# Performance work log

Measured on AMD Instinct MI355X. Metric: run time of the kernel, lower is better.

## Reference

```python
import jax, jax.numpy as jnp
import numpy as np

B, S, D_IN, D_CODE, K = 8, 4096, 1024, 64, 4096


def setup_inputs() -> dict:
    key = jax.random.key(0)
    k1, k2, k3, k4 = jax.random.split(key, 4)
    return {
        "input": jax.random.normal(k1, (B, S, D_IN), dtype=jnp.float32),
        "W_send": jax.random.normal(k2, (D_IN, D_CODE), dtype=jnp.float32) * (1.0 / np.sqrt(D_IN)),
        "b_send": jnp.zeros((D_CODE,), dtype=jnp.float32),
        "emb": jax.random.normal(k3, (K, D_CODE), dtype=jnp.float32),
        "W_recv": jax.random.normal(k4, (D_CODE, D_IN), dtype=jnp.float32) * (1.0 / np.sqrt(D_CODE)),
        "b_recv": jnp.zeros((D_IN,), dtype=jnp.float32),
    }


def reference(input, W_send, b_send, emb, W_recv, b_recv):
    # encoder: z = send(input) -> [B, S, D_CODE]
    z = jnp.einsum('bsi,ic->bsc', input, W_send) + b_send

    # VQEmbedding.lookup: argmin_k ||e_k||^2 - 2 <z, e_k>  (no-grad path)
    sqr = jnp.sum(emb * emb, axis=1)                      # [K]
    cov = jnp.einsum('bsc,kc->bsk', z, emb)               # [B, S, K]
    indices = jnp.argmin(sqr - 2.0 * cov, axis=-1)        # [B, S] int

    # fetch embeddings (gather)
    vectors = emb[indices]                                # [B, S, D_CODE]

    # straight-through estimator: values = z + sg(vectors - z)
    values = z + jax.lax.stop_gradient(vectors - z)

    # decoder: x = recv(values) -> [B, S, D_IN]
    x = jnp.einsum('bsc,ci->bsi', values, W_recv) + b_recv

    # VQEmbedding.loss (reduction='sum')
    embedding_loss = jnp.sum((vectors - jax.lax.stop_gradient(z)) ** 2)
    commitment_loss = jnp.sum((z - jax.lax.stop_gradient(vectors)) ** 2)

    # empirical code entropy in bits
    num_codes = emb.shape[0]
    counts = jnp.bincount(indices.ravel(), length=num_codes)
    p = counts.astype(jnp.float32) / jnp.float32(indices.size)
    ent = -jnp.sum(jnp.where(p > 0, p * jnp.log(jnp.where(p > 0, p, 1.0)), 0.0)) / jnp.log(2.0)

    return x, indices, embedding_loss, commitment_loss, ent
```

## Files before the change

kernel.cpp:

```cpp
#include <hip/hip_runtime.h>

#define DIN 1024
#define DC 64
#define KC 4096

typedef _Float16 f16x8 __attribute__((ext_vector_type(8)));
typedef _Float16 f16x4 __attribute__((ext_vector_type(4)));
typedef float f32x4 __attribute__((ext_vector_type(4)));

__device__ __forceinline__ void gll16(const void* g, void* l) {
    __builtin_amdgcn_global_load_lds(
        (const __attribute__((address_space(1))) unsigned int*)g,
        (__attribute__((address_space(3))) unsigned int*)l, 16, 0, 0);
}

__global__ __launch_bounds__(256) void k_prep(const float* __restrict__ emb,
                                              const float* __restrict__ Ws,
                                              const float* __restrict__ Wr,
                                              _Float16* __restrict__ Ee,
                                              float* __restrict__ sqr,
                                              _Float16* __restrict__ Wh,
                                              _Float16* __restrict__ WrT,
                                              int* __restrict__ counts) {
    int b = blockIdx.x;
    int tid = threadIdx.x;
    if (b < 1024) {
        int code = b * 4 + (tid >> 6);
        int lane = tid & 63;
        float v = emb[(size_t)code * DC + lane];
        Ee[(size_t)code * 64 + lane] = (_Float16)v;
        float s = v * v;
        #pragma unroll
        for (int m = 1; m < 64; m <<= 1) s += __shfl_xor(s, m);
        if (lane == 0) sqr[code] = s;
        if (tid < 4) counts[b * 4 + tid] = 0;
        return;
    }
    if (b < 1040) {
        int k0 = (b - 1024) * 64;
        #pragma unroll
        for (int it = 0; it < 16; ++it) {
            int q = it * 256 + tid;
            int c = q >> 6, kl = q & 63;
            float v = Ws[(size_t)(k0 + kl) * 64 + c];
            Wh[(size_t)c * 1024 + k0 + kl] = (_Float16)v;
        }
        return;
    }
    int b2 = b - 1040;
    #pragma unroll
    for (int it = 0; it < 16; ++it) {
        int k = it * 4 + (tid >> 6);
        int rr = b2 * 64 + (tid & 63);
        WrT[(size_t)rr * 64 + k] = (_Float16)Wr[(size_t)k * 1024 + rr];
    }
}

__global__ __launch_bounds__(256) void k_main(const float* __restrict__ in,
                                              const _Float16* __restrict__ Wh,
                                              const float* __restrict__ bs,
                                              const _Float16* __restrict__ Ee,
                                              const float* __restrict__ sqr,
                                              int* __restrict__ idx,
                                              float* __restrict__ out_idx,
                                              int* __restrict__ counts,
                                              float* __restrict__ lpart) {
    __shared__ char smem[32768];
    const int tid = threadIdx.x;
    const int row0 = blockIdx.x * 64;
    const int wid = tid >> 6, lane = tid & 63;
    const int c15 = lane & 15, g = lane >> 4;
    const int g16 = g * 16;
    const int wm = wid >> 1, wn = wid & 1;

    f32x4 acc[2][2];
    const f32x4 zz4 = {0.f, 0.f, 0.f, 0.f};
    #pragma unroll
    for (int mf = 0; mf < 2; ++mf)
        #pragma unroll
        for (int nf = 0; nf < 2; ++nf) acc[mf][nf] = zz4;

    int abyte[2], aswz[2], bbyte[2], bswz[2];
    #pragma unroll
    for (int mf = 0; mf < 2; ++mf) {
        int r = wm * 32 + mf * 16 + c15;
        abyte[mf] = r * 128; aswz[mf] = (r & 7) << 4;
    }
    #pragma unroll
    for (int nf = 0; nf < 2; ++nf) {
        int c = wn * 32 + nf * 16 + c15;
        bbyte[nf] = c * 128; bswz[nf] = (c & 7) << 4;
    }

    auto stageB = [&](int buf, int s) {
        char* dst = smem + buf * 16384 + 8192;
        #pragma unroll
        for (int r = 0; r < 2; ++r) {
            int p = r * 4096 + wid * 1024 + lane * 16;
            int row = p >> 7, off = p & 127;
            int soff = off ^ ((row & 7) << 4);
            gll16((const char*)Wh + (size_t)row * 2048 + s * 128 + soff,
                  dst + p);
        }
    };
    auto loadA = [&](int s, float4* a) {
        #pragma unroll
        for (int it = 0; it < 4; ++it) {
            int q = it * 256 + tid;
            int r = q >> 4, c4 = q & 15;
            a[it] = *(const float4*)&in[(size_t)(row0 + r) * DIN + s * 64 + c4 * 4];
        }
    };
    auto writeA = [&](int buf, const float4* a) {
        char* Ah = smem + buf * 16384;
        #pragma unroll
        for (int it = 0; it < 4; ++it) {
            int q = it * 256 + tid;
            int r = q >> 4, c4 = q & 15;
            float v[4] = {a[it].x, a[it].y, a[it].z, a[it].w};
            f16x4 h;
            #pragma unroll
            for (int j = 0; j < 4; ++j) h[j] = (_Float16)v[j];
            int o = r * 128 + ((c4 * 8) ^ ((r & 7) << 4));
            *(f16x4*)(Ah + o) = h;
        }
    };
    auto compute = [&](int buf) {
        const char* Ah = smem + buf * 16384;
        const char* Bh = Ah + 8192;
        #pragma unroll
        for (int ks = 0; ks < 2; ++ks) {
            int koff = ks * 64 + g16;
            f16x8 bh[2];
            #pragma unroll
            for (int nf = 0; nf < 2; ++nf)
                bh[nf] = *(const f16x8*)(Bh + bbyte[nf] + (koff ^ bswz[nf]));
            #pragma unroll
            for (int mf = 0; mf < 2; ++mf) {
                f16x8 ah = *(const f16x8*)(Ah + abyte[mf] + (koff ^ aswz[mf]));
                #pragma unroll
                for (int nf = 0; nf < 2; ++nf)
                    acc[mf][nf] = __builtin_amdgcn_mfma_f32_16x16x32_f16(
                        ah, bh[nf], acc[mf][nf], 0, 0, 0);
            }
        }
    };

    {
        float4 a0[4];
        loadA(0, a0);
        stageB(0, 0);
        writeA(0, a0);
    }
    __syncthreads();
    for (int s = 0; s < 16; ++s) {
        int c = s & 1;
        float4 an[4];
        if (s < 15) {
            loadA(s + 1, an);
            stageB(c ^ 1, s + 1);
        }
        compute(c);
        if (s < 15) writeA(c ^ 1, an);
        __syncthreads();
    }

    char* Zt = smem + 16384;
    #pragma unroll
    for (int nf = 0; nf < 2; ++nf) {
        int k = wn * 32 + nf * 16 + c15;
        float bias = bs[k];
        #pragma unroll
        for (int mf = 0; mf < 2; ++mf)
            #pragma unroll
            for (int r2 = 0; r2 < 4; ++r2) {
                int row = wm * 32 + mf * 16 + g * 4 + r2;
                _Float16 zh = (_Float16)(acc[mf][nf][r2] + bias);
                *(_Float16*)(Zt + row * 128 + ((k * 2) ^ ((row & 7) << 4))) = zh;
            }
    }
    __syncthreads();

    const int wm2 = wm, wn2 = wn;
    f16x8 zfh[2][2];
    #pragma unroll
    for (int nf = 0; nf < 2; ++nf) {
        int zr = wn2 * 32 + nf * 16 + c15;
        int sw = (zr & 7) << 4;
        #pragma unroll
        for (int j = 0; j < 2; ++j)
            zfh[j][nf] = *(const f16x8*)(Zt + zr * 128 + ((j * 64 + g16) ^ sw));
    }

    int rbase[2], rx[2];
    #pragma unroll
    for (int mf = 0; mf < 2; ++mf) {
        int r = wm2 * 32 + mf * 16 + c15;
        rbase[mf] = r * 128;
        rx[mf] = (r & 7) << 4;
    }

    auto stageE = [&](int ch, int buf) {
        char* dst = smem + buf * 8192;
        const char* src = (const char*)Ee + (size_t)ch * 8192;
        #pragma unroll
        for (int t = 0; t < 2; ++t) {
            int p = t * 4096 + tid * 16;
            int r = p >> 7, off = p & 127;
            gll16(src + r * 128 + (off ^ ((r & 7) << 4)), dst + p);
        }
    };

    float bv[2];
    int   bi[2];
    #pragma unroll
    for (int nf = 0; nf < 2; ++nf) { bv[nf] = 3.402823466e38f; bi[nf] = 0; }

    stageE(0, 0);
    __syncthreads();

    for (int ch = 0; ch < 64; ++ch) {
        const int buf = ch & 1;
        f32x4 sqv[2];
        #pragma unroll
        for (int mf = 0; mf < 2; ++mf)
            sqv[mf] = *(const f32x4*)(sqr + ch * 64 + wm2 * 32 + mf * 16 + g * 4);

        if (ch < 63) stageE(ch + 1, buf ^ 1);

        const char* base = smem + buf * 8192;
        f32x4 sacc[2][2];
        #pragma unroll
        for (int j = 0; j < 2; ++j) {
            const int kbyte = j * 64 + g16;
            f16x8 af[2];
            #pragma unroll
            for (int mf = 0; mf < 2; ++mf)
                af[mf] = *(const f16x8*)(base + rbase[mf] + (kbyte ^ rx[mf]));
            #pragma unroll
            for (int mf = 0; mf < 2; ++mf)
                #pragma unroll
                for (int nf = 0; nf < 2; ++nf)
                    sacc[mf][nf] = __builtin_amdgcn_mfma_f32_16x16x32_f16(
                        af[mf], zfh[j][nf],
                        j == 0 ? zz4 : sacc[mf][nf], 0, 0, 0);
        }

        #pragma unroll
        for (int nf = 0; nf < 2; ++nf) {
            #pragma unroll
            for (int mf = 0; mf < 2; ++mf) {
                f32x4 v = sqv[mf] - sacc[mf][nf] * 2.0f;
                #pragma unroll
                for (int r2 = 0; r2 < 4; ++r2) {
                    if (v[r2] < bv[nf]) {
                        bv[nf] = v[r2];
                        bi[nf] = ch * 64 + wm2 * 32 + mf * 16 + g * 4 + r2;
                    }
                }
            }
        }
        __syncthreads();
    }

    float* redv = (float*)(smem + 24576);
    int*   redi = (int*)(smem + 25088);
    float* zsqa = (float*)(smem + 25600);

    #pragma unroll
    for (int nf = 0; nf < 2; ++nf) {
        float v_ = bv[nf]; int i_ = bi[nf];
        #pragma unroll
        for (int m = 16; m <= 32; m <<= 1) {
            float ov = __shfl_xor(v_, m);
            int oi = __shfl_xor(i_, m);
            if (ov < v_ || (ov == v_ && oi < i_)) { v_ = ov; i_ = oi; }
        }
        if (g == 0) {
            int rl = wn2 * 32 + nf * 16 + c15;
            redv[wm2 * 64 + rl] = v_;
            redi[wm2 * 64 + rl] = i_;
        }
    }
    if (wm2 == 0) {
        #pragma unroll
        for (int nf = 0; nf < 2; ++nf) {
            float s = 0.f;
            #pragma unroll
            for (int j = 0; j < 2; ++j)
                #pragma unroll
                for (int e = 0; e < 8; ++e) {
                    float zv = (float)zfh[j][nf][e];
                    s += zv * zv;
                }
            s += __shfl_xor(s, 16);
            s += __shfl_xor(s, 32);
            if (g == 0) zsqa[wn2 * 32 + nf * 16 + c15] = s;
        }
    }
    __syncthreads();
    if (tid < 64) {
        float v0 = redv[tid]; int i0 = redi[tid];
        float v1 = redv[64 + tid]; int i1 = redi[64 + tid];
        if (v1 < v0 || (v1 == v0 && i1 < i0)) { v0 = v1; i0 = i1; }
        int grow = row0 + tid;
        idx[grow] = i0;
        out_idx[grow] = (float)i0;
        atomicAdd(&counts[i0], 1);
        float lossv = v0 + zsqa[tid];
        #pragma unroll
        for (int m = 1; m < 64; m <<= 1) lossv += __shfl_xor(lossv, m);
        if (tid == 0) lpart[blockIdx.x] = lossv;
    }
}

__global__ __launch_bounds__(256) void k_recv(const _Float16* __restrict__ Ee,
                                              const _Float16* __restrict__ WrT,
                                              const float* __restrict__ br,
                                              const int* __restrict__ idx,
                                              const int* __restrict__ counts,
                                              const float* __restrict__ lpart,
                                              float* __restrict__ x,
                                              float* __restrict__ out_sc) {
    __shared__ char smem[24832];
    int tid = threadIdx.x;

    if (blockIdx.x == 512) {
        float* red = (float*)smem;
        red[tid] = lpart[tid] + lpart[256 + tid];
        __syncthreads();
        for (int s = 128; s > 0; s >>= 1) {
            if (tid < s) red[tid] += red[tid + s];
            __syncthreads();
        }
        float loss = red[0];
        __syncthreads();
        float ep = 0.f;
        for (int k = tid; k < KC; k += 256) {
            int c = counts[k];
            if (c > 0) {
                float p = (float)c / 32768.0f;
                ep += p * logf(p);
            }
        }
        red[tid] = ep; __syncthreads();
        for (int s = 128; s > 0; s >>= 1) {
            if (tid < s) red[tid] += red[tid + s];
            __syncthreads();
        }
        if (tid == 0) {
            out_sc[0] = loss;
            out_sc[1] = loss;
            out_sc[2] = -red[0] * 1.4426950408889634f;
        }
        return;
    }

    const int row0 = blockIdx.x * 64;
    const int wid = tid >> 6, lane = tid & 63;
    const int c15 = lane & 15, g = lane >> 4;
    const int g16 = g * 16;
    int* sidx = (int*)(smem + 24576);

    if (tid < 64) sidx[tid] = idx[row0 + tid];
    __syncthreads();

    #pragma unroll
    for (int t = 0; t < 2; ++t) {
        int p = t * 4096 + tid * 16;
        int r = p >> 7, off = p & 127;
        gll16((const char*)Ee + (size_t)sidx[r] * 128 + (off ^ ((r & 7) << 4)),
              smem + p);
    }

    auto stageW = [&](int cc, int buf) {
        char* dst = smem + 8192 + buf * 8192;
        #pragma unroll
        for (int t = 0; t < 2; ++t) {
            int p = t * 4096 + tid * 16;
            int r = p >> 7, off = p & 127;
            gll16((const char*)WrT + (size_t)(cc * 64 + r) * 128
                      + (off ^ ((r & 7) << 4)),
                  dst + p);
        }
    };
    stageW(0, 0);
    __syncthreads();

    int abase[4], ax[4];
    #pragma unroll
    for (int mf = 0; mf < 4; ++mf) {
        int r = mf * 16 + c15;
        abase[mf] = r * 128;
        ax[mf] = (r & 7) << 4;
    }
    const int brow = wid * 16 + c15;
    const int bbase = 8192 + brow * 128;
    const int bx = (brow & 7) << 4;

    const f32x4 zz4 = {0.f, 0.f, 0.f, 0.f};
    for (int cc = 0; cc < 16; ++cc) {
        const int buf = cc & 1;
        if (cc < 15) stageW(cc + 1, buf ^ 1);

        const int col = cc * 64 + wid * 16 + c15;
        float bias = br[col];

        f32x4 acc[4];
        #pragma unroll
        for (int j = 0; j < 2; ++j) {
            const int kbyte = j * 64 + g16;
            f16x8 bf = *(const f16x8*)(smem + buf * 8192 + bbase + (kbyte ^ bx));
            #pragma unroll
            for (int mf = 0; mf < 4; ++mf) {
                f16x8 af = *(const f16x8*)(smem + abase[mf] + (kbyte ^ ax[mf]));
                acc[mf] = __builtin_amdgcn_mfma_f32_16x16x32_f16(
                    af, bf, j == 0 ? zz4 : acc[mf], 0, 0, 0);
            }
        }

        #pragma unroll
        for (int mf = 0; mf < 4; ++mf)
            #pragma unroll
            for (int r2 = 0; r2 < 4; ++r2)
                x[(size_t)(row0 + mf * 16 + g * 4 + r2) * DIN + col]
                    = acc[mf][r2] + bias;

        __syncthreads();
    }
}

extern "C" void kernel_launch(void* const* d_in, const int* in_sizes, int n_in,
                              void* d_out, int out_size, void* d_ws, size_t ws_size,
                              hipStream_t stream) {
    (void)in_sizes; (void)n_in; (void)out_size; (void)ws_size;
    const float* input  = (const float*)d_in[0];
    const float* W_send = (const float*)d_in[1];
    const float* b_send = (const float*)d_in[2];
    const float* emb    = (const float*)d_in[3];
    const float* W_recv = (const float*)d_in[4];
    const float* b_recv = (const float*)d_in[5];
    float* out = (float*)d_out;

    char* ws = (char*)d_ws;
    _Float16* Ee  = (_Float16*)(ws);
    float*    sqr = (float*)(ws + 524288);
    int*      idx = (int*)  (ws + 540672);
    int*   counts = (int*)  (ws + 671744);
    float* lpart  = (float*)(ws + 688128);
    _Float16* Wh  = (_Float16*)(ws + 690176);
    _Float16* WrT = (_Float16*)(ws + 821248);

    float* out_x   = out;
    float* out_idx = out + 33554432;
    float* out_sc  = out + 33587200;

    k_prep<<<1056, 256, 0, stream>>>(emb, W_send, W_recv, Ee, sqr, Wh, WrT, counts);
    k_main<<<512, 256, 0, stream>>>(input, Wh, b_send, Ee, sqr,
                                    idx, out_idx, counts, lpart);
    k_recv<<<513, 256, 0, stream>>>(Ee, WrT, b_recv, idx, counts, lpart,
                                    out_x, out_sc);
}
```

Baseline: 91.01 us.

## Split fused encoder/codebook-scoring kernel into separate send and score kernels

The fused main kernel is split in two. The encoder GEMM now writes z as fp16 to a global workspace buffer, and a new 512-thread scoring kernel reads it back and searches the codebook in 128-code chunks using 8 waves. Each kernel can then use its own block shape and occupancy (launch_bounds 512,4 for scoring), which is meant to raise parallelism in the argmin phase. The cost is an extra launch plus a global round trip for z (about 4 MB) instead of keeping it in shared memory.

```diff
diff --git a/kernel.cpp b/kernel.cpp
--- a/kernel.cpp
+++ b/kernel.cpp
@@ -56,29 +56,23 @@
     }
 }
 
-__global__ __launch_bounds__(256) void k_main(const float* __restrict__ in,
+__global__ __launch_bounds__(256) void k_send(const float* __restrict__ in,
                                               const _Float16* __restrict__ Wh,
                                               const float* __restrict__ bs,
-                                              const _Float16* __restrict__ Ee,
-                                              const float* __restrict__ sqr,
-                                              int* __restrict__ idx,
-                                              float* __restrict__ out_idx,
-                                              int* __restrict__ counts,
-                                              float* __restrict__ lpart) {
+                                              _Float16* __restrict__ Ze) {
     __shared__ char smem[32768];
     const int tid = threadIdx.x;
     const int row0 = blockIdx.x * 64;
     const int wid = tid >> 6, lane = tid & 63;
     const int c15 = lane & 15, g = lane >> 4;
-    const int g16 = g * 16;
     const int wm = wid >> 1, wn = wid & 1;
 
     f32x4 acc[2][2];
-    const f32x4 zz4 = {0.f, 0.f, 0.f, 0.f};
+    const f32x4 z4 = {0.f, 0.f, 0.f, 0.f};
     #pragma unroll
     for (int mf = 0; mf < 2; ++mf)
         #pragma unroll
-        for (int nf = 0; nf < 2; ++nf) acc[mf][nf] = zz4;
+        for (int nf = 0; nf < 2; ++nf) acc[mf][nf] = z4;
 
     int abyte[2], aswz[2], bbyte[2], bswz[2];
     #pragma unroll
@@ -91,6 +85,7 @@
         int c = wn * 32 + nf * 16 + c15;
         bbyte[nf] = c * 128; bswz[nf] = (c & 7) << 4;
     }
+    const int g16 = g * 16;
 
     auto stageB = [&](int buf, int s) {
         char* dst = smem + buf * 16384 + 8192;
@@ -103,6 +98,7 @@
                   dst + p);
         }
     };
+
     auto loadA = [&](int s, float4* a) {
         #pragma unroll
         for (int it = 0; it < 4; ++it) {
@@ -111,6 +107,7 @@
             a[it] = *(const float4*)&in[(size_t)(row0 + r) * DIN + s * 64 + c4 * 4];
         }
     };
+
     auto writeA = [&](int buf, const float4* a) {
         char* Ah = smem + buf * 16384;
         #pragma unroll
@@ -125,6 +122,7 @@
             *(f16x4*)(Ah + o) = h;
         }
     };
+
     auto compute = [&](int buf) {
         const char* Ah = smem + buf * 16384;
         const char* Bh = Ah + 8192;
@@ -153,6 +151,7 @@
         writeA(0, a0);
     }
     __syncthreads();
+
     for (int s = 0; s < 16; ++s) {
         int c = s & 1;
         float4 an[4];
@@ -165,49 +164,63 @@
         __syncthreads();
     }
 
-    char* Zt = smem + 16384;
     #pragma unroll
     for (int nf = 0; nf < 2; ++nf) {
-        int k = wn * 32 + nf * 16 + c15;
-        float bias = bs[k];
-        #pragma unroll
-        for (int mf = 0; mf < 2; ++mf)
+        int col = wn * 32 + nf * 16 + c15;
+        float bias = bs[col];
+        #pragma unroll
+        for (int mf = 0; mf < 2; ++mf) {
             #pragma unroll
             for (int r2 = 0; r2 < 4; ++r2) {
-                int row = wm * 32 + mf * 16 + g * 4 + r2;
-                _Float16 zh = (_Float16)(acc[mf][nf][r2] + bias);
-                *(_Float16*)(Zt + row * 128 + ((k * 2) ^ ((row & 7) << 4))) = zh;
+                float zv = acc[mf][nf][r2] + bias;
+                int row = row0 + wm * 32 + mf * 16 + g * 4 + r2;
+                Ze[(size_t)row * 64 + col] = (_Float16)zv;
             }
-    }
-    __syncthreads();
-
-    const int wm2 = wm, wn2 = wn;
+        }
+    }
+}
+
+__global__ __launch_bounds__(512, 4) void k_score(const _Float16* __restrict__ Ee,
+                                                  const _Float16* __restrict__ Ze,
+                                                  const float* __restrict__ sqr,
+                                                  int* __restrict__ idx,
+                                                  float* __restrict__ out_idx,
+                                                  int* __restrict__ counts,
+                                                  float* __restrict__ lpart) {
+    __shared__ char smem[35072];
+    const int tid = threadIdx.x;
+    const int row0 = blockIdx.x * 64;
+    const int wid = tid >> 6, lane = tid & 63;
+    const int c15 = lane & 15, g = lane >> 4;
+    const int wm = wid >> 1;
+    const int wn = wid & 1;
+    const int g16 = g * 16;
+
     f16x8 zfh[2][2];
     #pragma unroll
     for (int nf = 0; nf < 2; ++nf) {
-        int zr = wn2 * 32 + nf * 16 + c15;
-        int sw = (zr & 7) << 4;
+        const _Float16* zr = Ze + (size_t)(row0 + wn * 32 + nf * 16 + c15) * 64;
         #pragma unroll
         for (int j = 0; j < 2; ++j)
-            zfh[j][nf] = *(const f16x8*)(Zt + zr * 128 + ((j * 64 + g16) ^ sw));
+            zfh[j][nf] = *(const f16x8*)(zr + j * 32 + g * 8);
     }
 
     int rbase[2], rx[2];
     #pragma unroll
     for (int mf = 0; mf < 2; ++mf) {
-        int r = wm2 * 32 + mf * 16 + c15;
+        int r = wm * 32 + mf * 16 + c15;
         rbase[mf] = r * 128;
         rx[mf] = (r & 7) << 4;
     }
 
-    auto stageE = [&](int ch, int buf) {
-        char* dst = smem + buf * 8192;
-        const char* src = (const char*)Ee + (size_t)ch * 8192;
+    auto stage = [&](int ch, int buf) {
+        char* dst = smem + buf * 16384;
+        const char* src = (const char*)Ee + (size_t)ch * 16384;
         #pragma unroll
         for (int t = 0; t < 2; ++t) {
-            int p = t * 4096 + tid * 16;
-            int r = p >> 7, off = p & 127;
-            gll16(src + r * 128 + (off ^ ((r & 7) << 4)), dst + p);
+            int p = t * 8192 + tid * 16;
+            int r = p >> 7, b = p & 127;
+            gll16(src + r * 128 + (b ^ ((r & 7) << 4)), dst + p);
         }
     };
 
@@ -216,20 +229,22 @@
     #pragma unroll
     for (int nf = 0; nf < 2; ++nf) { bv[nf] = 3.402823466e38f; bi[nf] = 0; }
 
-    stageE(0, 0);
+    const f32x4 zz4 = {0.f, 0.f, 0.f, 0.f};
+
+    stage(0, 0);
     __syncthreads();
 
-    for (int ch = 0; ch < 64; ++ch) {
+    for (int ch = 0; ch < 32; ++ch) {
         const int buf = ch & 1;
         f32x4 sqv[2];
         #pragma unroll
         for (int mf = 0; mf < 2; ++mf)
-            sqv[mf] = *(const f32x4*)(sqr + ch * 64 + wm2 * 32 + mf * 16 + g * 4);
-
-        if (ch < 63) stageE(ch + 1, buf ^ 1);
-
-        const char* base = smem + buf * 8192;
-        f32x4 sacc[2][2];
+            sqv[mf] = *(const f32x4*)(sqr + ch * 128 + wm * 32 + mf * 16 + g * 4);
+
+        if (ch < 31) stage(ch + 1, buf ^ 1);
+
+        const char* base = smem + buf * 16384;
+        f32x4 acc[2][2];
         #pragma unroll
         for (int j = 0; j < 2; ++j) {
             const int kbyte = j * 64 + g16;
@@ -241,21 +256,21 @@
             for (int mf = 0; mf < 2; ++mf)
                 #pragma unroll
                 for (int nf = 0; nf < 2; ++nf)
-                    sacc[mf][nf] = __builtin_amdgcn_mfma_f32_16x16x32_f16(
+                    acc[mf][nf] = __builtin_amdgcn_mfma_f32_16x16x32_f16(
                         af[mf], zfh[j][nf],
-                        j == 0 ? zz4 : sacc[mf][nf], 0, 0, 0);
+                        j == 0 ? zz4 : acc[mf][nf], 0, 0, 0);
         }
 
         #pragma unroll
         for (int nf = 0; nf < 2; ++nf) {
             #pragma unroll
             for (int mf = 0; mf < 2; ++mf) {
-                f32x4 v = sqv[mf] - sacc[mf][nf] * 2.0f;
+                f32x4 v = sqv[mf] - acc[mf][nf] * 2.0f;
                 #pragma unroll
                 for (int r2 = 0; r2 < 4; ++r2) {
                     if (v[r2] < bv[nf]) {
                         bv[nf] = v[r2];
-                        bi[nf] = ch * 64 + wm2 * 32 + mf * 16 + g * 4 + r2;
+                        bi[nf] = ch * 128 + wm * 32 + mf * 16 + g * 4 + r2;
                     }
                 }
             }
@@ -263,9 +278,9 @@
         __syncthreads();
     }
 
-    float* redv = (float*)(smem + 24576);
-    int*   redi = (int*)(smem + 25088);
-    float* zsqa = (float*)(smem + 25600);
+    float* redv = (float*)(smem + 32768);
+    int*   redi = (int*)(smem + 33792);
+    float* zsqa = (float*)(smem + 34816);
 
     #pragma unroll
     for (int nf = 0; nf < 2; ++nf) {
@@ -277,12 +292,12 @@
             if (ov < v_ || (ov == v_ && oi < i_)) { v_ = ov; i_ = oi; }
         }
         if (g == 0) {
-            int rl = wn2 * 32 + nf * 16 + c15;
-            redv[wm2 * 64 + rl] = v_;
-            redi[wm2 * 64 + rl] = i_;
-        }
-    }
-    if (wm2 == 0) {
+            int rl = wn * 32 + nf * 16 + c15;
+            redv[wm * 64 + rl] = v_;
+            redi[wm * 64 + rl] = i_;
+        }
+    }
+    if (wm == 0) {
         #pragma unroll
         for (int nf = 0; nf < 2; ++nf) {
             float s = 0.f;
@@ -295,14 +310,17 @@
                 }
             s += __shfl_xor(s, 16);
             s += __shfl_xor(s, 32);
-            if (g == 0) zsqa[wn2 * 32 + nf * 16 + c15] = s;
+            if (g == 0) zsqa[wn * 32 + nf * 16 + c15] = s;
         }
     }
     __syncthreads();
     if (tid < 64) {
         float v0 = redv[tid]; int i0 = redi[tid];
-        float v1 = redv[64 + tid]; int i1 = redi[64 + tid];
-        if (v1 < v0 || (v1 == v0 && i1 < i0)) { v0 = v1; i0 = i1; }
+        #pragma unroll
+        for (int w = 1; w < 4; ++w) {
+            float v1 = redv[w * 64 + tid]; int i1 = redi[w * 64 + tid];
+            if (v1 < v0 || (v1 == v0 && i1 < i0)) { v0 = v1; i0 = i1; }
+        }
         int grow = row0 + tid;
         idx[grow] = i0;
         out_idx[grow] = (float)i0;
@@ -443,21 +461,22 @@
     float* out = (float*)d_out;
 
     char* ws = (char*)d_ws;
-    _Float16* Ee  = (_Float16*)(ws);
-    float*    sqr = (float*)(ws + 524288);
-    int*      idx = (int*)  (ws + 540672);
-    int*   counts = (int*)  (ws + 671744);
-    float* lpart  = (float*)(ws + 688128);
-    _Float16* Wh  = (_Float16*)(ws + 690176);
-    _Float16* WrT = (_Float16*)(ws + 821248);
+    _Float16* Ze  = (_Float16*)(ws);
+    _Float16* Ee  = (_Float16*)(ws + 4194304);
+    float*    sqr = (float*)(ws + 4718592);
+    int*      idx = (int*)  (ws + 4734976);
+    int*   counts = (int*)  (ws + 4866048);
+    float* lpart  = (float*)(ws + 4882432);
+    _Float16* Wh  = (_Float16*)(ws + 4884480);
+    _Float16* WrT = (_Float16*)(ws + 5015552);
 
     float* out_x   = out;
     float* out_idx = out + 33554432;
     float* out_sc  = out + 33587200;
 
     k_prep<<<1056, 256, 0, stream>>>(emb, W_send, W_recv, Ee, sqr, Wh, WrT, counts);
-    k_main<<<512, 256, 0, stream>>>(input, Wh, b_send, Ee, sqr,
-                                    idx, out_idx, counts, lpart);
+    k_send<<<512, 256, 0, stream>>>(input, Wh, b_send, Ze);
+    k_score<<<512, 512, 0, stream>>>(Ee, Ze, sqr, idx, out_idx, counts, lpart);
     k_recv<<<513, 256, 0, stream>>>(Ee, WrT, b_recv, idx, counts, lpart,
                                     out_x, out_sc);
 }
```

New measurement: 95.28 us. 1.05x slower.

## Use 512-thread blocks with larger K-steps and codebook chunks in k_main

Applied to the files above, without the earlier changes.

Doubles k_main's block to 8 waves and enlarges the encoder K-step from 64 to 128 columns, cutting the loop to 8 iterations. Codebook chunks staged in LDS grow from 64 to 256 codes, giving 16 iterations with 4 M-fragments per wave. Work is split over 4 row-groups, and the argmin reduction now merges 4 partial results. This reduces barrier count and per-chunk overhead but raises LDS use to about 74 KB per block, which may limit occupancy.

```diff
diff --git a/kernel.cpp b/kernel.cpp
--- a/kernel.cpp
+++ b/kernel.cpp
@@ -56,93 +56,84 @@
     }
 }
 
-__global__ __launch_bounds__(256) void k_main(const float* __restrict__ in,
-                                              const _Float16* __restrict__ Wh,
-                                              const float* __restrict__ bs,
-                                              const _Float16* __restrict__ Ee,
-                                              const float* __restrict__ sqr,
-                                              int* __restrict__ idx,
-                                              float* __restrict__ out_idx,
-                                              int* __restrict__ counts,
-                                              float* __restrict__ lpart) {
-    __shared__ char smem[32768];
+__global__ __launch_bounds__(512, 2) void k_main(const float* __restrict__ in,
+                                                 const _Float16* __restrict__ Wh,
+                                                 const float* __restrict__ bs,
+                                                 const _Float16* __restrict__ Ee,
+                                                 const float* __restrict__ sqr,
+                                                 int* __restrict__ idx,
+                                                 float* __restrict__ out_idx,
+                                                 int* __restrict__ counts,
+                                                 float* __restrict__ lpart) {
+    __shared__ char smem[76032];
     const int tid = threadIdx.x;
     const int row0 = blockIdx.x * 64;
     const int wid = tid >> 6, lane = tid & 63;
     const int c15 = lane & 15, g = lane >> 4;
     const int g16 = g * 16;
     const int wm = wid >> 1, wn = wid & 1;
-
-    f32x4 acc[2][2];
     const f32x4 zz4 = {0.f, 0.f, 0.f, 0.f};
-    #pragma unroll
-    for (int mf = 0; mf < 2; ++mf)
-        #pragma unroll
-        for (int nf = 0; nf < 2; ++nf) acc[mf][nf] = zz4;
-
-    int abyte[2], aswz[2], bbyte[2], bswz[2];
-    #pragma unroll
-    for (int mf = 0; mf < 2; ++mf) {
-        int r = wm * 32 + mf * 16 + c15;
-        abyte[mf] = r * 128; aswz[mf] = (r & 7) << 4;
-    }
+
+    f32x4 acc[2];
+    acc[0] = zz4; acc[1] = zz4;
+
+    int abyte, aswz;
+    { int r = wm * 16 + c15; abyte = r * 256; aswz = (r & 7) << 4; }
+    int bbyte[2], bswz[2];
     #pragma unroll
     for (int nf = 0; nf < 2; ++nf) {
         int c = wn * 32 + nf * 16 + c15;
-        bbyte[nf] = c * 128; bswz[nf] = (c & 7) << 4;
+        bbyte[nf] = c * 256; bswz[nf] = (c & 7) << 4;
     }
 
     auto stageB = [&](int buf, int s) {
-        char* dst = smem + buf * 16384 + 8192;
-        #pragma unroll
-        for (int r = 0; r < 2; ++r) {
-            int p = r * 4096 + wid * 1024 + lane * 16;
-            int row = p >> 7, off = p & 127;
-            int soff = off ^ ((row & 7) << 4);
-            gll16((const char*)Wh + (size_t)row * 2048 + s * 128 + soff,
+        char* dst = smem + buf * 32768 + 16384;
+        #pragma unroll
+        for (int t = 0; t < 2; ++t) {
+            int p = t * 8192 + tid * 16;
+            int row = p >> 8, off = p & 255;
+            gll16((const char*)Wh + (size_t)row * 2048 + s * 256
+                      + (off ^ ((row & 7) << 4)),
                   dst + p);
         }
     };
     auto loadA = [&](int s, float4* a) {
         #pragma unroll
         for (int it = 0; it < 4; ++it) {
-            int q = it * 256 + tid;
-            int r = q >> 4, c4 = q & 15;
-            a[it] = *(const float4*)&in[(size_t)(row0 + r) * DIN + s * 64 + c4 * 4];
+            int q = it * 512 + tid;
+            int r = q >> 5, c4 = q & 31;
+            a[it] = *(const float4*)&in[(size_t)(row0 + r) * DIN + s * 128 + c4 * 4];
         }
     };
     auto writeA = [&](int buf, const float4* a) {
-        char* Ah = smem + buf * 16384;
+        char* Ah = smem + buf * 32768;
         #pragma unroll
         for (int it = 0; it < 4; ++it) {
-            int q = it * 256 + tid;
-            int r = q >> 4, c4 = q & 15;
+            int q = it * 512 + tid;
+            int r = q >> 5, c4 = q & 31;
             float v[4] = {a[it].x, a[it].y, a[it].z, a[it].w};
             f16x4 h;
             #pragma unroll
             for (int j = 0; j < 4; ++j) h[j] = (_Float16)v[j];
-            int o = r * 128 + ((c4 * 8) ^ ((r & 7) << 4));
+            int o = r * 256 + ((c4 * 8) ^ ((r & 7) << 4));
             *(f16x4*)(Ah + o) = h;
         }
     };
-    auto compute = [&](int buf) {
-        const char* Ah = smem + buf * 16384;
-        const char* Bh = Ah + 8192;
-        #pragma unroll
-        for (int ks = 0; ks < 2; ++ks) {
+    auto computeS = [&](int buf) {
+        const char* Ah = smem + buf * 32768;
+        const char* Bh = Ah + 16384;
+        #pragma unroll
+        for (int ks = 0; ks < 4; ++ks) {
             int koff = ks * 64 + g16;
             f16x8 bh[2];
             #pragma unroll
             for (int nf = 0; nf < 2; ++nf)
                 bh[nf] = *(const f16x8*)(Bh + bbyte[nf] + (koff ^ bswz[nf]));
-            #pragma unroll
-            for (int mf = 0; mf < 2; ++mf) {
-                f16x8 ah = *(const f16x8*)(Ah + abyte[mf] + (koff ^ aswz[mf]));
-                #pragma unroll
-                for (int nf = 0; nf < 2; ++nf)
-                    acc[mf][nf] = __builtin_amdgcn_mfma_f32_16x16x32_f16(
-                        ah, bh[nf], acc[mf][nf], 0, 0, 0);
-            }
+            f16x8 ah = *(const f16x8*)(Ah + abyte + (koff ^ aswz));
+            #pragma unroll
+            for (int nf = 0; nf < 2; ++nf)
+                acc[nf] = __builtin_amdgcn_mfma_f32_16x16x32_f16(
+                    ah, bh[nf], acc[nf], 0, 0, 0);
         }
     };
 
@@ -153,92 +144,87 @@
         writeA(0, a0);
     }
     __syncthreads();
-    for (int s = 0; s < 16; ++s) {
+    for (int s = 0; s < 8; ++s) {
         int c = s & 1;
         float4 an[4];
-        if (s < 15) {
+        if (s < 7) {
             loadA(s + 1, an);
             stageB(c ^ 1, s + 1);
         }
-        compute(c);
-        if (s < 15) writeA(c ^ 1, an);
+        computeS(c);
+        if (s < 7) writeA(c ^ 1, an);
         __syncthreads();
     }
 
-    char* Zt = smem + 16384;
+    char* Zt = smem + 65536;
     #pragma unroll
     for (int nf = 0; nf < 2; ++nf) {
-        int k = wn * 32 + nf * 16 + c15;
-        float bias = bs[k];
-        #pragma unroll
-        for (int mf = 0; mf < 2; ++mf)
-            #pragma unroll
-            for (int r2 = 0; r2 < 4; ++r2) {
-                int row = wm * 32 + mf * 16 + g * 4 + r2;
-                _Float16 zh = (_Float16)(acc[mf][nf][r2] + bias);
-                *(_Float16*)(Zt + row * 128 + ((k * 2) ^ ((row & 7) << 4))) = zh;
-            }
-    }
+        int col = wn * 32 + nf * 16 + c15;
+        float bias = bs[col];
+        #pragma unroll
+        for (int r2 = 0; r2 < 4; ++r2) {
+            int row = wm * 16 + g * 4 + r2;
+            *(_Float16*)(Zt + row * 128 + ((col * 2) ^ ((row & 7) << 4)))
+                = (_Float16)(acc[nf][r2] + bias);
+        }
+    }
+
+    auto stageE = [&](int ch, int buf) {
+        char* dst = smem + buf * 32768;
+        const char* src = (const char*)Ee + (size_t)ch * 32768;
+        #pragma unroll
+        for (int t = 0; t < 4; ++t) {
+            int p = t * 8192 + tid * 16;
+            int r = p >> 7, off = p & 127;
+            gll16(src + r * 128 + (off ^ ((r & 7) << 4)), dst + p);
+        }
+    };
+    stageE(0, 0);
     __syncthreads();
 
-    const int wm2 = wm, wn2 = wn;
     f16x8 zfh[2][2];
     #pragma unroll
     for (int nf = 0; nf < 2; ++nf) {
-        int zr = wn2 * 32 + nf * 16 + c15;
+        int zr = wn * 32 + nf * 16 + c15;
         int sw = (zr & 7) << 4;
         #pragma unroll
         for (int j = 0; j < 2; ++j)
             zfh[j][nf] = *(const f16x8*)(Zt + zr * 128 + ((j * 64 + g16) ^ sw));
     }
 
-    int rbase[2], rx[2];
-    #pragma unroll
-    for (int mf = 0; mf < 2; ++mf) {
-        int r = wm2 * 32 + mf * 16 + c15;
+    int rbase[4], rx[4];
+    #pragma unroll
+    for (int mf = 0; mf < 4; ++mf) {
+        int r = wm * 64 + mf * 16 + c15;
         rbase[mf] = r * 128;
         rx[mf] = (r & 7) << 4;
     }
 
-    auto stageE = [&](int ch, int buf) {
-        char* dst = smem + buf * 8192;
-        const char* src = (const char*)Ee + (size_t)ch * 8192;
-        #pragma unroll
-        for (int t = 0; t < 2; ++t) {
-            int p = t * 4096 + tid * 16;
-            int r = p >> 7, off = p & 127;
-            gll16(src + r * 128 + (off ^ ((r & 7) << 4)), dst + p);
-        }
-    };
-
     float bv[2];
     int   bi[2];
     #pragma unroll
     for (int nf = 0; nf < 2; ++nf) { bv[nf] = 3.402823466e38f; bi[nf] = 0; }
 
-    stageE(0, 0);
-    __syncthreads();
-
-    for (int ch = 0; ch < 64; ++ch) {
+    for (int ch = 0; ch < 16; ++ch) {
         const int buf = ch & 1;
-        f32x4 sqv[2];
-        #pragma unroll
-        for (int mf = 0; mf < 2; ++mf)
-            sqv[mf] = *(const f32x4*)(sqr + ch * 64 + wm2 * 32 + mf * 16 + g * 4);
-
-        if (ch < 63) stageE(ch + 1, buf ^ 1);
-
-        const char* base = smem + buf * 8192;
-        f32x4 sacc[2][2];
+        f32x4 sqv[4];
+        #pragma unroll
+        for (int mf = 0; mf < 4; ++mf)
+            sqv[mf] = *(const f32x4*)(sqr + ch * 256 + wm * 64 + mf * 16 + g * 4);
+
+        if (ch < 15) stageE(ch + 1, buf ^ 1);
+
+        const char* base = smem + buf * 32768;
+        f32x4 sacc[4][2];
         #pragma unroll
         for (int j = 0; j < 2; ++j) {
             const int kbyte = j * 64 + g16;
-            f16x8 af[2];
-            #pragma unroll
-            for (int mf = 0; mf < 2; ++mf)
+            f16x8 af[4];
+            #pragma unroll
+            for (int mf = 0; mf < 4; ++mf)
                 af[mf] = *(const f16x8*)(base + rbase[mf] + (kbyte ^ rx[mf]));
             #pragma unroll
-            for (int mf = 0; mf < 2; ++mf)
+            for (int mf = 0; mf < 4; ++mf)
                 #pragma unroll
                 for (int nf = 0; nf < 2; ++nf)
                     sacc[mf][nf] = __builtin_amdgcn_mfma_f32_16x16x32_f16(
@@ -249,13 +235,13 @@
         #pragma unroll
         for (int nf = 0; nf < 2; ++nf) {
             #pragma unroll
-            for (int mf = 0; mf < 2; ++mf) {
+            for (int mf = 0; mf < 4; ++mf) {
                 f32x4 v = sqv[mf] - sacc[mf][nf] * 2.0f;
                 #pragma unroll
                 for (int r2 = 0; r2 < 4; ++r2) {
                     if (v[r2] < bv[nf]) {
                         bv[nf] = v[r2];
-                        bi[nf] = ch * 64 + wm2 * 32 + mf * 16 + g * 4 + r2;
+                        bi[nf] = ch * 256 + wm * 64 + mf * 16 + g * 4 + r2;
                     }
                 }
             }
@@ -263,9 +249,9 @@
         __syncthreads();
     }
 
-    float* redv = (float*)(smem + 24576);
-    int*   redi = (int*)(smem + 25088);
-    float* zsqa = (float*)(smem + 25600);
+    float* redv = (float*)(smem + 73728);
+    int*   redi = (int*)(smem + 74752);
+    float* zsqa = (float*)(smem + 75776);
 
     #pragma unroll
     for (int nf = 0; nf < 2; ++nf) {
@@ -277,12 +263,12 @@
             if (ov < v_ || (ov == v_ && oi < i_)) { v_ = ov; i_ = oi; }
         }
         if (g == 0) {
-            int rl = wn2 * 32 + nf * 16 + c15;
-            redv[wm2 * 64 + rl] = v_;
-            redi[wm2 * 64 + rl] = i_;
-        }
-    }
-    if (wm2 == 0) {
+            int rl = wn * 32 + nf * 16 + c15;
+            redv[wm * 64 + rl] = v_;
+            redi[wm * 64 + rl] = i_;
+        }
+    }
+    if (wm == 0) {
         #pragma unroll
         for (int nf = 0; nf < 2; ++nf) {
             float s = 0.f;
@@ -295,14 +281,17 @@
                 }
             s += __shfl_xor(s, 16);
             s += __shfl_xor(s, 32);
-            if (g == 0) zsqa[wn2 * 32 + nf * 16 + c15] = s;
+            if (g == 0) zsqa[wn * 32 + nf * 16 + c15] = s;
         }
     }
     __syncthreads();
     if (tid < 64) {
         float v0 = redv[tid]; int i0 = redi[tid];
-        float v1 = redv[64 + tid]; int i1 = redi[64 + tid];
-        if (v1 < v0 || (v1 == v0 && i1 < i0)) { v0 = v1; i0 = i1; }
+        #pragma unroll
+        for (int w = 1; w < 4; ++w) {
+            float v1 = redv[w * 64 + tid]; int i1 = redi[w * 64 + tid];
+            if (v1 < v0 || (v1 == v0 && i1 < i0)) { v0 = v1; i0 = i1; }
+        }
         int grow = row0 + tid;
         idx[grow] = i0;
         out_idx[grow] = (float)i0;
@@ -456,7 +445,7 @@
     float* out_sc  = out + 33587200;
 
     k_prep<<<1056, 256, 0, stream>>>(emb, W_send, W_recv, Ee, sqr, Wh, WrT, counts);
-    k_main<<<512, 256, 0, stream>>>(input, Wh, b_send, Ee, sqr,
+    k_main<<<512, 512, 0, stream>>>(input, Wh, b_send, Ee, sqr,
                                     idx, out_idx, counts, lpart);
     k_recv<<<513, 256, 0, stream>>>(Ee, WrT, b_recv, idx, counts, lpart,
                                     out_x, out_sc);
```

Measured after the change: 95.06 us. 4.5% more time.

## Fuse VQ encoder/argmin kernel with decoder GEMM into one kernel

Applied to the files above, without the earlier changes.

Merges the encode+argmin kernel with the decode kernel so each block takes its 64 rows from encoder through lookup to decoder output. The chosen indices stay in shared memory instead of going out to global memory and being read back. The first W_recv tile is prefetched during the argmin reduction, and the scalar loss/entropy reduction moves into a separate single-block kernel. This removes one full-size kernel launch and the idx round trip. In exchange the fused kernel is longer and may use more registers per block.

```diff
diff --git a/kernel.cpp b/kernel.cpp
--- a/kernel.cpp
+++ b/kernel.cpp
@@ -56,15 +56,17 @@
     }
 }
 
-__global__ __launch_bounds__(256) void k_main(const float* __restrict__ in,
-                                              const _Float16* __restrict__ Wh,
-                                              const float* __restrict__ bs,
-                                              const _Float16* __restrict__ Ee,
-                                              const float* __restrict__ sqr,
-                                              int* __restrict__ idx,
-                                              float* __restrict__ out_idx,
-                                              int* __restrict__ counts,
-                                              float* __restrict__ lpart) {
+__global__ __launch_bounds__(256) void k_all(const float* __restrict__ in,
+                                             const _Float16* __restrict__ Wh,
+                                             const float* __restrict__ bs,
+                                             const _Float16* __restrict__ Ee,
+                                             const float* __restrict__ sqr,
+                                             const _Float16* __restrict__ WrT,
+                                             const float* __restrict__ br,
+                                             float* __restrict__ x,
+                                             float* __restrict__ out_idx,
+                                             int* __restrict__ counts,
+                                             float* __restrict__ lpart) {
     __shared__ char smem[32768];
     const int tid = threadIdx.x;
     const int row0 = blockIdx.x * 64;
@@ -72,9 +74,9 @@
     const int c15 = lane & 15, g = lane >> 4;
     const int g16 = g * 16;
     const int wm = wid >> 1, wn = wid & 1;
+    const f32x4 zz4 = {0.f, 0.f, 0.f, 0.f};
 
     f32x4 acc[2][2];
-    const f32x4 zz4 = {0.f, 0.f, 0.f, 0.f};
     #pragma unroll
     for (int mf = 0; mf < 2; ++mf)
         #pragma unroll
@@ -125,7 +127,7 @@
             *(f16x4*)(Ah + o) = h;
         }
     };
-    auto compute = [&](int buf) {
+    auto computeS = [&](int buf) {
         const char* Ah = smem + buf * 16384;
         const char* Bh = Ah + 8192;
         #pragma unroll
@@ -160,7 +162,7 @@
             loadA(s + 1, an);
             stageB(c ^ 1, s + 1);
         }
-        compute(c);
+        computeS(c);
         if (s < 15) writeA(c ^ 1, an);
         __syncthreads();
     }
@@ -175,29 +177,9 @@
             #pragma unroll
             for (int r2 = 0; r2 < 4; ++r2) {
                 int row = wm * 32 + mf * 16 + g * 4 + r2;
-                _Float16 zh = (_Float16)(acc[mf][nf][r2] + bias);
-                *(_Float16*)(Zt + row * 128 + ((k * 2) ^ ((row & 7) << 4))) = zh;
+                *(_Float16*)(Zt + row * 128 + ((k * 2) ^ ((row & 7) << 4)))
+                    = (_Float16)(acc[mf][nf][r2] + bias);
             }
-    }
-    __syncthreads();
-
-    const int wm2 = wm, wn2 = wn;
-    f16x8 zfh[2][2];
-    #pragma unroll
-    for (int nf = 0; nf < 2; ++nf) {
-        int zr = wn2 * 32 + nf * 16 + c15;
-        int sw = (zr & 7) << 4;
-        #pragma unroll
-        for (int j = 0; j < 2; ++j)
-            zfh[j][nf] = *(const f16x8*)(Zt + zr * 128 + ((j * 64 + g16) ^ sw));
-    }
-
-    int rbase[2], rx[2];
-    #pragma unroll
-    for (int mf = 0; mf < 2; ++mf) {
-        int r = wm2 * 32 + mf * 16 + c15;
-        rbase[mf] = r * 128;
-        rx[mf] = (r & 7) << 4;
     }
 
     auto stageE = [&](int ch, int buf) {
@@ -210,21 +192,38 @@
             gll16(src + r * 128 + (off ^ ((r & 7) << 4)), dst + p);
         }
     };
+    stageE(0, 0);
+    __syncthreads();
+
+    f16x8 zfh[2][2];
+    #pragma unroll
+    for (int nf = 0; nf < 2; ++nf) {
+        int zr = wn * 32 + nf * 16 + c15;
+        int sw = (zr & 7) << 4;
+        #pragma unroll
+        for (int j = 0; j < 2; ++j)
+            zfh[j][nf] = *(const f16x8*)(Zt + zr * 128 + ((j * 64 + g16) ^ sw));
+    }
+
+    int rbase[2], rx[2];
+    #pragma unroll
+    for (int mf = 0; mf < 2; ++mf) {
+        int r = wm * 32 + mf * 16 + c15;
+        rbase[mf] = r * 128;
+        rx[mf] = (r & 7) << 4;
+    }
 
     float bv[2];
     int   bi[2];
     #pragma unroll
     for (int nf = 0; nf < 2; ++nf) { bv[nf] = 3.402823466e38f; bi[nf] = 0; }
-
-    stageE(0, 0);
-    __syncthreads();
 
     for (int ch = 0; ch < 64; ++ch) {
         const int buf = ch & 1;
         f32x4 sqv[2];
         #pragma unroll
         for (int mf = 0; mf < 2; ++mf)
-            sqv[mf] = *(const f32x4*)(sqr + ch * 64 + wm2 * 32 + mf * 16 + g * 4);
+            sqv[mf] = *(const f32x4*)(sqr + ch * 64 + wm * 32 + mf * 16 + g * 4);
 
         if (ch < 63) stageE(ch + 1, buf ^ 1);
 
@@ -255,7 +254,7 @@
                 for (int r2 = 0; r2 < 4; ++r2) {
                     if (v[r2] < bv[nf]) {
                         bv[nf] = v[r2];
-                        bi[nf] = ch * 64 + wm2 * 32 + mf * 16 + g * 4 + r2;
+                        bi[nf] = ch * 64 + wm * 32 + mf * 16 + g * 4 + r2;
                     }
                 }
             }
@@ -263,9 +262,23 @@
         __syncthreads();
     }
 
+    auto stageW = [&](int cc, int buf) {
+        char* dst = smem + buf * 8192;
+        #pragma unroll
+        for (int t = 0; t < 2; ++t) {
+            int p = t * 4096 + tid * 16;
+            int r = p >> 7, off = p & 127;
+            gll16((const char*)WrT + (size_t)(cc * 64 + r) * 128
+                      + (off ^ ((r & 7) << 4)),
+                  dst + p);
+        }
+    };
+    stageW(0, 0);
+
     float* redv = (float*)(smem + 24576);
     int*   redi = (int*)(smem + 25088);
     float* zsqa = (float*)(smem + 25600);
+    int*   sidx = (int*)(smem + 25856);
 
     #pragma unroll
     for (int nf = 0; nf < 2; ++nf) {
@@ -277,12 +290,12 @@
             if (ov < v_ || (ov == v_ && oi < i_)) { v_ = ov; i_ = oi; }
         }
         if (g == 0) {
-            int rl = wn2 * 32 + nf * 16 + c15;
-            redv[wm2 * 64 + rl] = v_;
-            redi[wm2 * 64 + rl] = i_;
-        }
-    }
-    if (wm2 == 0) {
+            int rl = wn * 32 + nf * 16 + c15;
+            redv[wm * 64 + rl] = v_;
+            redi[wm * 64 + rl] = i_;
+        }
+    }
+    if (wm == 0) {
         #pragma unroll
         for (int nf = 0; nf < 2; ++nf) {
             float s = 0.f;
@@ -295,7 +308,7 @@
                 }
             s += __shfl_xor(s, 16);
             s += __shfl_xor(s, 32);
-            if (g == 0) zsqa[wn2 * 32 + nf * 16 + c15] = s;
+            if (g == 0) zsqa[wn * 32 + nf * 16 + c15] = s;
         }
     }
     __syncthreads();
@@ -304,65 +317,14 @@
         float v1 = redv[64 + tid]; int i1 = redi[64 + tid];
         if (v1 < v0 || (v1 == v0 && i1 < i0)) { v0 = v1; i0 = i1; }
         int grow = row0 + tid;
-        idx[grow] = i0;
         out_idx[grow] = (float)i0;
+        sidx[tid] = i0;
         atomicAdd(&counts[i0], 1);
         float lossv = v0 + zsqa[tid];
         #pragma unroll
         for (int m = 1; m < 64; m <<= 1) lossv += __shfl_xor(lossv, m);
         if (tid == 0) lpart[blockIdx.x] = lossv;
     }
-}
-
-__global__ __launch_bounds__(256) void k_recv(const _Float16* __restrict__ Ee,
-                                              const _Float16* __restrict__ WrT,
-                                              const float* __restrict__ br,
-                                              const int* __restrict__ idx,
-                                              const int* __restrict__ counts,
-                                              const float* __restrict__ lpart,
-                                              float* __restrict__ x,
-                                              float* __restrict__ out_sc) {
-    __shared__ char smem[24832];
-    int tid = threadIdx.x;
-
-    if (blockIdx.x == 512) {
-        float* red = (float*)smem;
-        red[tid] = lpart[tid] + lpart[256 + tid];
-        __syncthreads();
-        for (int s = 128; s > 0; s >>= 1) {
-            if (tid < s) red[tid] += red[tid + s];
-            __syncthreads();
-        }
-        float loss = red[0];
-        __syncthreads();
-        float ep = 0.f;
-        for (int k = tid; k < KC; k += 256) {
-            int c = counts[k];
-            if (c > 0) {
-                float p = (float)c / 32768.0f;
-                ep += p * logf(p);
-            }
-        }
-        red[tid] = ep; __syncthreads();
-        for (int s = 128; s > 0; s >>= 1) {
-            if (tid < s) red[tid] += red[tid + s];
-            __syncthreads();
-        }
-        if (tid == 0) {
-            out_sc[0] = loss;
-            out_sc[1] = loss;
-            out_sc[2] = -red[0] * 1.4426950408889634f;
-        }
-        return;
-    }
-
-    const int row0 = blockIdx.x * 64;
-    const int wid = tid >> 6, lane = tid & 63;
-    const int c15 = lane & 15, g = lane >> 4;
-    const int g16 = g * 16;
-    int* sidx = (int*)(smem + 24576);
-
-    if (tid < 64) sidx[tid] = idx[row0 + tid];
     __syncthreads();
 
     #pragma unroll
@@ -370,35 +332,21 @@
         int p = t * 4096 + tid * 16;
         int r = p >> 7, off = p & 127;
         gll16((const char*)Ee + (size_t)sidx[r] * 128 + (off ^ ((r & 7) << 4)),
-              smem + p);
-    }
-
-    auto stageW = [&](int cc, int buf) {
-        char* dst = smem + 8192 + buf * 8192;
-        #pragma unroll
-        for (int t = 0; t < 2; ++t) {
-            int p = t * 4096 + tid * 16;
-            int r = p >> 7, off = p & 127;
-            gll16((const char*)WrT + (size_t)(cc * 64 + r) * 128
-                      + (off ^ ((r & 7) << 4)),
-                  dst + p);
-        }
-    };
-    stageW(0, 0);
-    __syncthreads();
-
-    int abase[4], ax[4];
+              smem + 16384 + p);
+    }
+    __syncthreads();
+
+    int rabase[4], rax[4];
     #pragma unroll
     for (int mf = 0; mf < 4; ++mf) {
         int r = mf * 16 + c15;
-        abase[mf] = r * 128;
-        ax[mf] = (r & 7) << 4;
+        rabase[mf] = 16384 + r * 128;
+        rax[mf] = (r & 7) << 4;
     }
     const int brow = wid * 16 + c15;
-    const int bbase = 8192 + brow * 128;
+    const int bbase = brow * 128;
     const int bx = (brow & 7) << 4;
 
-    const f32x4 zz4 = {0.f, 0.f, 0.f, 0.f};
     for (int cc = 0; cc < 16; ++cc) {
         const int buf = cc & 1;
         if (cc < 15) stageW(cc + 1, buf ^ 1);
@@ -406,16 +354,16 @@
         const int col = cc * 64 + wid * 16 + c15;
         float bias = br[col];
 
-        f32x4 acc[4];
+        f32x4 racc[4];
         #pragma unroll
         for (int j = 0; j < 2; ++j) {
             const int kbyte = j * 64 + g16;
             f16x8 bf = *(const f16x8*)(smem + buf * 8192 + bbase + (kbyte ^ bx));
             #pragma unroll
             for (int mf = 0; mf < 4; ++mf) {
-                f16x8 af = *(const f16x8*)(smem + abase[mf] + (kbyte ^ ax[mf]));
-                acc[mf] = __builtin_amdgcn_mfma_f32_16x16x32_f16(
-                    af, bf, j == 0 ? zz4 : acc[mf], 0, 0, 0);
+                f16x8 af = *(const f16x8*)(smem + rabase[mf] + (kbyte ^ rax[mf]));
+                racc[mf] = __builtin_amdgcn_mfma_f32_16x16x32_f16(
+                    af, bf, j == 0 ? zz4 : racc[mf], 0, 0, 0);
             }
         }
 
@@ -424,9 +372,44 @@
             #pragma unroll
             for (int r2 = 0; r2 < 4; ++r2)
                 x[(size_t)(row0 + mf * 16 + g * 4 + r2) * DIN + col]
-                    = acc[mf][r2] + bias;
+                    = racc[mf][r2] + bias;
 
         __syncthreads();
+    }
+}
+
+__global__ __launch_bounds__(256) void k_final(const int* __restrict__ counts,
+                                               const float* __restrict__ lpart,
+                                               float* __restrict__ out_sc) {
+    __shared__ float red[256];
+    int tid = threadIdx.x;
+
+    red[tid] = lpart[tid] + lpart[256 + tid];
+    __syncthreads();
+    for (int s = 128; s > 0; s >>= 1) {
+        if (tid < s) red[tid] += red[tid + s];
+        __syncthreads();
+    }
+    float loss = red[0];
+    __syncthreads();
+
+    float ep = 0.f;
+    for (int k = tid; k < KC; k += 256) {
+        int c = counts[k];
+        if (c > 0) {
+            float p = (float)c / 32768.0f;
+            ep += p * logf(p);
+        }
+    }
+    red[tid] = ep; __syncthreads();
+    for (int s = 128; s > 0; s >>= 1) {
+        if (tid < s) red[tid] += red[tid + s];
+        __syncthreads();
+    }
+    if (tid == 0) {
+        out_sc[0] = loss;
+        out_sc[1] = loss;
+        out_sc[2] = -red[0] * 1.4426950408889634f;
     }
 }
 
@@ -445,7 +428,6 @@
     char* ws = (char*)d_ws;
     _Float16* Ee  = (_Float16*)(ws);
     float*    sqr = (float*)(ws + 524288);
-    int*      idx = (int*)  (ws + 540672);
     int*   counts = (int*)  (ws + 671744);
     float* lpart  = (float*)(ws + 688128);
     _Float16* Wh  = (_Float16*)(ws + 690176);
@@ -456,8 +438,7 @@
     float* out_sc  = out + 33587200;
 
     k_prep<<<1056, 256, 0, stream>>>(emb, W_send, W_recv, Ee, sqr, Wh, WrT, counts);
-    k_main<<<512, 256, 0, stream>>>(input, Wh, b_send, Ee, sqr,
-                                    idx, out_idx, counts, lpart);
-    k_recv<<<513, 256, 0, stream>>>(Ee, WrT, b_recv, idx, counts, lpart,
-                                    out_x, out_sc);
+    k_all<<<512, 256, 0, stream>>>(input, Wh, b_send, Ee, sqr, WrT, b_recv,
+                                   out_x, out_idx, counts, lpart);
+    k_final<<<1, 256, 0, stream>>>(counts, lpart, out_sc);
 }
```

After: 96.58 us. 1.06x slower.
